# Performance work log

Hardware: AMD Instinct MI355X
Metric: run time of the kernel (lower is better)

Reference implementation:

```python
import jax, jax.numpy as jnp
import numpy as np

B, S, D, H, HS = 2, 2048, 1024, 16, 64


def setup_inputs() -> dict:
    key = jax.random.key(0)
    ks = jax.random.split(key, 4)
    x = jax.random.normal(ks[0], (B, S, D), dtype=jnp.float32)
    # causal mask: 1.0 where key_pos <= query_pos, else 0.0
    mask = jnp.tril(jnp.ones((S, S), dtype=jnp.float32))
    w_qkv = jax.random.normal(ks[1], (D, 3, H, HS), dtype=jnp.float32) * 0.02
    b_qkv = jnp.zeros((3, H, HS), dtype=jnp.float32)
    w_proj = jax.random.normal(ks[2], (H, HS, D), dtype=jnp.float32) * 0.02
    b_proj = jnp.zeros((D,), dtype=jnp.float32)
    return {"x": x, "mask": mask, "w_qkv": w_qkv, "b_qkv": b_qkv,
            "w_proj": w_proj, "b_proj": b_proj}


def reference(x, mask, w_qkv, b_qkv, w_proj, b_proj):
    # c_attn: [B,S,D] @ [D,3,H,HS] -> [B,S,3,H,HS]
    qkv = jnp.einsum('bsd,dthc->bsthc', x, w_qkv) + b_qkv
    q, k, v = qkv[:, :, 0], qkv[:, :, 1], qkv[:, :, 2]  # [B,S,H,HS]
    scale = jax.lax.rsqrt(float(HS))
    q = q * scale
    # scores over head_size: [B,H,S(query),S(key)]
    scores = jnp.einsum('bqhc,bkhc->bhqk', q, k)
    scores = scores + (1.0 - mask) * -1e9
    weights = jax.nn.softmax(scores, axis=-1).astype(x.dtype)
    # attn_pdrop = 0.0 / inference: dropout is identity
    attn = jnp.einsum('bhqk,bkhc->bqhc', weights, v)  # [B,S,H,HS]
    out = jnp.einsum('bqhc,hcd->bqd', attn, w_proj) + b_proj
    return out
```

## Files before the change

### kernel.cpp

```cpp
#include <hip/hip_runtime.h>
#include <hip/hip_bf16.h>


#define Bb 2
#define Ss 2048
#define Dd 1024
#define Hh 16
#define HSs 64

typedef __bf16 bf16x8 __attribute__((ext_vector_type(8)));
typedef float  f32x4  __attribute__((ext_vector_type(4)));

__device__ __forceinline__ unsigned short f2bf(float f) {
  unsigned int u = __float_as_uint(f);
  unsigned int lsb = (u >> 16) & 1u;
  u += 0x7fffu + lsb;
  return (unsigned short)(u >> 16);
}

__device__ __forceinline__ void async16(const unsigned short* g, unsigned short* l) {
  __builtin_amdgcn_global_load_lds(
      (const __attribute__((address_space(1))) unsigned int*)g,
      (__attribute__((address_space(3))) unsigned int*)l,
      16, 0, 0);
}

__global__ __launch_bounds__(256) void k_cvt_bf16(const float* __restrict__ in,
                                                  unsigned short* __restrict__ out,
                                                  int n) {
  int i = (blockIdx.x * 256 + threadIdx.x) * 4;
  int stride = gridDim.x * 256 * 4;
  for (; i < n; i += stride) {
    float4 v = *reinterpret_cast<const float4*>(in + i);
    ushort4 o;
    o.x = f2bf(v.x); o.y = f2bf(v.y); o.z = f2bf(v.z); o.w = f2bf(v.w);
    *reinterpret_cast<ushort4*>(out + i) = o;
  }
}

__global__ __launch_bounds__(256) void k_transpose_bf16(const float* __restrict__ in,
                                                        unsigned short* __restrict__ out,
                                                        int R, int C) {
  __shared__ float t[32][33];
  int c0 = blockIdx.x * 32, r0 = blockIdx.y * 32;
  int tx = threadIdx.x, ty = threadIdx.y;
  #pragma unroll
  for (int i = 0; i < 32; i += 8)
    t[ty + i][tx] = in[(size_t)(r0 + ty + i) * C + (c0 + tx)];
  __syncthreads();
  #pragma unroll
  for (int i = 0; i < 32; i += 8)
    out[(size_t)(c0 + ty + i) * R + (r0 + tx)] = f2bf(t[tx][ty + i]);
}

__global__ __launch_bounds__(256) void k_gemm_qkv(const unsigned short* __restrict__ A,
                                                  const unsigned short* __restrict__ Bt,
                                                  const float* __restrict__ bias,
                                                  unsigned short* __restrict__ Qg,
                                                  unsigned short* __restrict__ Kg,
                                                  unsigned short* __restrict__ Vt) {
  __shared__ unsigned short As[128 * 64];
  __shared__ unsigned short Bs[128 * 64];
  const int K = 1024;
  int bid = blockIdx.x;
  int tm = bid / 24, tn = bid % 24;
  int m0 = tm * 128, n0 = tn * 128;
  int tid = threadIdx.x;
  int w = tid >> 6, l = tid & 63;
  int lr = l & 15, lg = l >> 4;
  int wm = (w >> 1) * 64, wn = (w & 1) * 64;
  int srow = l >> 3, scol = (l & 7) * 8;

  f32x4 acc[4][4];
  #pragma unroll
  for (int i = 0; i < 4; ++i)
    #pragma unroll
    for (int j = 0; j < 4; ++j)
      acc[i][j] = (f32x4){0.f, 0.f, 0.f, 0.f};

  for (int k0 = 0; k0 < K; k0 += 64) {
    #pragma unroll
    for (int c = 0; c < 4; ++c) {
      int chunk = w * 4 + c;
      int row = chunk * 8 + srow;
      async16(&A[(size_t)(m0 + row) * K + k0 + scol], &As[chunk * 512]);
      async16(&Bt[(size_t)(n0 + row) * K + k0 + scol], &Bs[chunk * 512]);
    }
    __syncthreads();
    #pragma unroll
    for (int kk = 0; kk < 64; kk += 32) {
      bf16x8 af[4], bfr[4];
      #pragma unroll
      for (int mf = 0; mf < 4; ++mf)
        af[mf] = *reinterpret_cast<const bf16x8*>(&As[(wm + mf * 16 + lr) * 64 + kk + lg * 8]);
      #pragma unroll
      for (int nf = 0; nf < 4; ++nf)
        bfr[nf] = *reinterpret_cast<const bf16x8*>(&Bs[(wn + nf * 16 + lr) * 64 + kk + lg * 8]);
      #pragma unroll
      for (int mf = 0; mf < 4; ++mf)
        #pragma unroll
        for (int nf = 0; nf < 4; ++nf)
          acc[mf][nf] = __builtin_amdgcn_mfma_f32_16x16x32_bf16(af[mf], bfr[nf], acc[mf][nf], 0, 0, 0);
    }
    __syncthreads();
  }

  #pragma unroll
  for (int mf = 0; mf < 4; ++mf) {
    #pragma unroll
    for (int nf = 0; nf < 4; ++nf) {
      int n = n0 + wn + nf * 16 + lr;
      int t = n >> 10, r = n & 1023;
      int h = r >> 6, cc = r & 63;
      float bv = bias[n];
      if (t == 2) {
        int m = m0 + wm + mf * 16 + lg * 4;
        int b = m >> 11, s = m & 2047;
        ushort4 pk;
        pk.x = f2bf(acc[mf][nf][0] + bv);
        pk.y = f2bf(acc[mf][nf][1] + bv);
        pk.z = f2bf(acc[mf][nf][2] + bv);
        pk.w = f2bf(acc[mf][nf][3] + bv);
        *reinterpret_cast<ushort4*>(&Vt[((size_t)(b * Hh + h) * HSs + cc) * Ss + s]) = pk;
      } else {
        #pragma unroll
        for (int j = 0; j < 4; ++j) {
          int m = m0 + wm + mf * 16 + lg * 4 + j;
          int b = m >> 11, s = m & 2047;
          size_t idx = ((size_t)(b * Hh + h) * Ss + s) * HSs + cc;
          float v = acc[mf][nf][j] + bv;
          if (t == 0) Qg[idx] = f2bf(v * 0.125f);
          else        Kg[idx] = f2bf(v);
        }
      }
    }
  }
}

__global__ __launch_bounds__(256, 4) void k_attn(const unsigned short* __restrict__ Qg,
                                                 const unsigned short* __restrict__ Kg,
                                                 const unsigned short* __restrict__ Vt,
                                                 unsigned short* __restrict__ Ob) {
  __shared__ unsigned short Ks[64 * 64];
  __shared__ unsigned short Vs[64 * 64];
  __shared__ unsigned short Ps[4][16 * 72];

  int bid = blockIdx.x;
  int xcd = bid & 7, slot = (bid >> 3) & 3, idx = bid >> 5;
  int bh = (idx & 3) * 8 + xcd;
  int base = (idx >> 2) * 2 + (slot & 1);
  int qt = (slot & 2) ? 31 - base : base;
  int b = bh >> 4, h = bh & 15;
  int qs0 = qt * 64;

  int tid = threadIdx.x;
  int w = tid >> 6, l = tid & 63;
  int lr = l & 15, lg = l >> 4;
  int qw = qs0 + w * 16;
  int srow = l >> 3, scol = (l & 7) * 8;
  int swcol = scol ^ (srow << 3);

  bf16x8 qf[2];
  #pragma unroll
  for (int kx = 0; kx < 2; ++kx)
    qf[kx] = *reinterpret_cast<const bf16x8*>(
        &Qg[((size_t)bh * Ss + qw + lr) * HSs + kx * 32 + lg * 8]);

  f32x4 oacc[4];
  #pragma unroll
  for (int nf = 0; nf < 4; ++nf) oacc[nf] = (f32x4){0.f, 0.f, 0.f, 0.f};
  float mrun[4], lrun[4];
  #pragma unroll
  for (int j = 0; j < 4; ++j) { mrun[j] = -1e30f; lrun[j] = 0.f; }

  int ntiles = qt + 1;
  for (int t = 0; t < ntiles; ++t) {
    #pragma unroll
    for (int cch = 0; cch < 2; ++cch) {
      int chunk = w * 2 + cch;
      int row = chunk * 8 + srow;
      async16(&Kg[((size_t)bh * Ss + t * 64 + row) * HSs + swcol], &Ks[chunk * 512]);
      async16(&Vt[((size_t)bh * HSs + row) * Ss + t * 64 + swcol], &Vs[chunk * 512]);
    }
    __syncthreads();

    f32x4 sacc[4];
    #pragma unroll
    for (int nf = 0; nf < 4; ++nf) sacc[nf] = (f32x4){0.f, 0.f, 0.f, 0.f};
    #pragma unroll
    for (int kx = 0; kx < 2; ++kx) {
      bf16x8 kf[4];
      #pragma unroll
      for (int nf = 0; nf < 4; ++nf)
        kf[nf] = *reinterpret_cast<const bf16x8*>(
            &Ks[(nf * 16 + lr) * 64 + ((kx * 32 + lg * 8) ^ ((lr & 7) << 3))]);
      #pragma unroll
      for (int nf = 0; nf < 4; ++nf)
        sacc[nf] = __builtin_amdgcn_mfma_f32_16x16x32_bf16(qf[kx], kf[nf], sacc[nf], 0, 0, 0);
    }

    if (t == ntiles - 1) {
      #pragma unroll
      for (int nf = 0; nf < 4; ++nf) {
        int kcol = qs0 + nf * 16 + lr;
        #pragma unroll
        for (int j = 0; j < 4; ++j) {
          int qg = qw + lg * 4 + j;
          if (kcol > qg) sacc[nf][j] = -1e30f;
        }
      }
    }

    #pragma unroll
    for (int j = 0; j < 4; ++j) {
      float rmax = fmaxf(fmaxf(sacc[0][j], sacc[1][j]), fmaxf(sacc[2][j], sacc[3][j]));
      #pragma unroll
      for (int d = 1; d < 16; d <<= 1)
        rmax = fmaxf(rmax, __shfl_xor(rmax, d));
      float mnew = fmaxf(mrun[j], rmax);
      float cf = __expf(mrun[j] - mnew);
      mrun[j] = mnew;
      float psum = 0.f;
      #pragma unroll
      for (int nf = 0; nf < 4; ++nf) {
        float p = __expf(sacc[nf][j] - mnew);
        sacc[nf][j] = p;
        psum += p;
      }
      #pragma unroll
      for (int d = 1; d < 16; d <<= 1)
        psum += __shfl_xor(psum, d);
      lrun[j] = lrun[j] * cf + psum;
      #pragma unroll
      for (int nf = 0; nf < 4; ++nf)
        oacc[nf][j] *= cf;
    }

    #pragma unroll
    for (int nf = 0; nf < 4; ++nf)
      #pragma unroll
      for (int j = 0; j < 4; ++j)
        Ps[w][(lg * 4 + j) * 72 + nf * 16 + lr] = f2bf(sacc[nf][j]);

    #pragma unroll
    for (int kx = 0; kx < 2; ++kx) {
      bf16x8 pf = *reinterpret_cast<const bf16x8*>(&Ps[w][lr * 72 + kx * 32 + lg * 8]);
      bf16x8 vf[4];
      #pragma unroll
      for (int nf = 0; nf < 4; ++nf)
        vf[nf] = *reinterpret_cast<const bf16x8*>(
            &Vs[(nf * 16 + lr) * 64 + ((kx * 32 + lg * 8) ^ ((lr & 7) << 3))]);
      #pragma unroll
      for (int nf = 0; nf < 4; ++nf)
        oacc[nf] = __builtin_amdgcn_mfma_f32_16x16x32_bf16(pf, vf[nf], oacc[nf], 0, 0, 0);
    }
    __syncthreads();
  }

  #pragma unroll
  for (int j = 0; j < 4; ++j) {
    float rinv = 1.0f / lrun[j];
    int s = qw + lg * 4 + j;
    #pragma unroll
    for (int nf = 0; nf < 4; ++nf) {
      int c = nf * 16 + lr;
      Ob[((size_t)(b * Ss + s)) * Dd + h * HSs + c] = f2bf(oacc[nf][j] * rinv);
    }
  }
}

__global__ __launch_bounds__(256) void k_gemm_out(const unsigned short* __restrict__ A,
                                                  const unsigned short* __restrict__ Bt,
                                                  const float* __restrict__ bias,
                                                  float* __restrict__ Out) {
  __shared__ unsigned short As[128 * 64];
  __shared__ unsigned short Bs[128 * 64];
  const int K = 1024;
  int bid = blockIdx.x;
  int tm = bid / 8, tn = bid % 8;
  int m0 = tm * 128, n0 = tn * 128;
  int tid = threadIdx.x;
  int w = tid >> 6, l = tid & 63;
  int lr = l & 15, lg = l >> 4;
  int wm = (w >> 1) * 64, wn = (w & 1) * 64;
  int srow = l >> 3, scol = (l & 7) * 8;

  f32x4 acc[4][4];
  #pragma unroll
  for (int i = 0; i < 4; ++i)
    #pragma unroll
    for (int j = 0; j < 4; ++j)
      acc[i][j] = (f32x4){0.f, 0.f, 0.f, 0.f};

  for (int k0 = 0; k0 < K; k0 += 64) {
    #pragma unroll
    for (int c = 0; c < 4; ++c) {
      int chunk = w * 4 + c;
      int row = chunk * 8 + srow;
      async16(&A[(size_t)(m0 + row) * K + k0 + scol], &As[chunk * 512]);
      async16(&Bt[(size_t)(n0 + row) * K + k0 + scol], &Bs[chunk * 512]);
    }
    __syncthreads();
    #pragma unroll
    for (int kk = 0; kk < 64; kk += 32) {
      bf16x8 af[4], bfr[4];
      #pragma unroll
      for (int mf = 0; mf < 4; ++mf)
        af[mf] = *reinterpret_cast<const bf16x8*>(&As[(wm + mf * 16 + lr) * 64 + kk + lg * 8]);
      #pragma unroll
      for (int nf = 0; nf < 4; ++nf)
        bfr[nf] = *reinterpret_cast<const bf16x8*>(&Bs[(wn + nf * 16 + lr) * 64 + kk + lg * 8]);
      #pragma unroll
      for (int mf = 0; mf < 4; ++mf)
        #pragma unroll
        for (int nf = 0; nf < 4; ++nf)
          acc[mf][nf] = __builtin_amdgcn_mfma_f32_16x16x32_bf16(af[mf], bfr[nf], acc[mf][nf], 0, 0, 0);
    }
    __syncthreads();
  }

  #pragma unroll
  for (int mf = 0; mf < 4; ++mf)
    #pragma unroll
    for (int nf = 0; nf < 4; ++nf) {
      int n = n0 + wn + nf * 16 + lr;
      float bv = bias[n];
      #pragma unroll
      for (int j = 0; j < 4; ++j) {
        int m = m0 + wm + mf * 16 + lg * 4 + j;
        Out[(size_t)m * 1024 + n] = acc[mf][nf][j] + bv;
      }
    }
}

extern "C" void kernel_launch(void* const* d_in, const int* in_sizes, int n_in,
                              void* d_out, int out_size, void* d_ws, size_t ws_size,
                              hipStream_t stream) {
  (void)in_sizes; (void)n_in; (void)out_size; (void)ws_size;
  const float* x      = (const float*)d_in[0];
  const float* w_qkv  = (const float*)d_in[2];
  const float* b_qkv  = (const float*)d_in[3];
  const float* w_proj = (const float*)d_in[4];
  const float* b_proj = (const float*)d_in[5];
  float* out = (float*)d_out;

  char* ws = (char*)d_ws;
  unsigned short* xb    = (unsigned short*)(ws);
  unsigned short* wqkvT = (unsigned short*)(ws + 8388608);
  unsigned short* wpT   = (unsigned short*)(ws + 14680064);
  unsigned short* Qg    = (unsigned short*)(ws + 16777216);
  unsigned short* Kg    = (unsigned short*)(ws + 25165824);
  unsigned short* Vt    = (unsigned short*)(ws + 33554432);
  unsigned short* attnb = (unsigned short*)(ws + 41943040);

  k_cvt_bf16<<<dim3(2048), dim3(256), 0, stream>>>(x, xb, Bb * Ss * Dd);
  k_transpose_bf16<<<dim3(96, 32), dim3(32, 8), 0, stream>>>(w_qkv, wqkvT, 1024, 3072);
  k_transpose_bf16<<<dim3(32, 32), dim3(32, 8), 0, stream>>>(w_proj, wpT, 1024, 1024);
  k_gemm_qkv<<<dim3(32 * 24), dim3(256), 0, stream>>>(xb, wqkvT, b_qkv, Qg, Kg, Vt);
  k_attn<<<dim3(1024), dim3(256), 0, stream>>>(Qg, Kg, Vt, attnb);
  k_gemm_out<<<dim3(32 * 8), dim3(256), 0, stream>>>(attnb, wpT, b_proj, out);
}
```

Baseline: 256.5 us.

## Pair causal query tiles per block with double-buffered K/V and XCD-swizzled GEMMs

The attention kernel now uses 512-thread blocks. Each block's two 4-wave groups handle complementary query tiles (p and 31-p), so every block runs an equal 32-p iterations and the K/V tiles loaded into LDS are shared by both groups. K/V loads are double-buffered so the next tile's async load overlaps the current tile's compute. Both GEMM kernels also remap block IDs so consecutive tiles land on the same XCD for L2 reuse. The cost is doubled LDS use, idle waves in the group whose tile finishes early, and a barrier shared by both groups.

```diff
diff --git a/kernel.cpp b/kernel.cpp
--- a/kernel.cpp
+++ b/kernel.cpp
@@ -63,7 +63,8 @@
   __shared__ unsigned short Bs[128 * 64];
   const int K = 1024;
   int bid = blockIdx.x;
-  int tm = bid / 24, tn = bid % 24;
+  int swz = (bid % 8) * 96 + bid / 8;
+  int tm = swz / 24, tn = swz % 24;
   int m0 = tm * 128, n0 = tn * 128;
   int tid = threadIdx.x;
   int w = tid >> 6, l = tid & 63;
@@ -137,26 +138,26 @@
   }
 }
 
-__global__ __launch_bounds__(256, 4) void k_attn(const unsigned short* __restrict__ Qg,
+__global__ __launch_bounds__(512, 4) void k_attn(const unsigned short* __restrict__ Qg,
                                                  const unsigned short* __restrict__ Kg,
                                                  const unsigned short* __restrict__ Vt,
                                                  unsigned short* __restrict__ Ob) {
-  __shared__ unsigned short Ks[64 * 64];
-  __shared__ unsigned short Vs[64 * 64];
-  __shared__ unsigned short Ps[4][16 * 72];
+  __shared__ unsigned short Ks[2][64 * 64];
+  __shared__ unsigned short Vs[2][64 * 64];
+  __shared__ unsigned short Ps[8][16 * 72];
 
   int bid = blockIdx.x;
-  int xcd = bid & 7, slot = (bid >> 3) & 3, idx = bid >> 5;
-  int bh = (idx & 3) * 8 + xcd;
-  int base = (idx >> 2) * 2 + (slot & 1);
-  int qt = (slot & 2) ? 31 - base : base;
+  int p  = bid >> 5;
+  int bh = bid & 31;
   int b = bh >> 4, h = bh & 15;
-  int qs0 = qt * 64;
 
   int tid = threadIdx.x;
   int w = tid >> 6, l = tid & 63;
+  int g = w >> 2;
+  int myqt = g ? (31 - p) : p;
+  int qs0 = myqt * 64;
   int lr = l & 15, lg = l >> 4;
-  int qw = qs0 + w * 16;
+  int qw = qs0 + (w & 3) * 16;
   int srow = l >> 3, scol = (l & 7) * 8;
   int swcol = scol ^ (srow << 3);
 
@@ -173,86 +174,93 @@
   #pragma unroll
   for (int j = 0; j < 4; ++j) { mrun[j] = -1e30f; lrun[j] = 0.f; }
 
-  int ntiles = qt + 1;
+  int ntiles = 32 - p;
+  {
+    int row = w * 8 + srow;
+    async16(&Kg[((size_t)bh * Ss + 0 * 64 + row) * HSs + swcol], &Ks[0][w * 512]);
+    async16(&Vt[((size_t)bh * HSs + row) * Ss + 0 * 64 + swcol], &Vs[0][w * 512]);
+  }
+  __syncthreads();
+
   for (int t = 0; t < ntiles; ++t) {
-    #pragma unroll
-    for (int cch = 0; cch < 2; ++cch) {
-      int chunk = w * 2 + cch;
-      int row = chunk * 8 + srow;
-      async16(&Kg[((size_t)bh * Ss + t * 64 + row) * HSs + swcol], &Ks[chunk * 512]);
-      async16(&Vt[((size_t)bh * HSs + row) * Ss + t * 64 + swcol], &Vs[chunk * 512]);
-    }
-    __syncthreads();
-
-    f32x4 sacc[4];
-    #pragma unroll
-    for (int nf = 0; nf < 4; ++nf) sacc[nf] = (f32x4){0.f, 0.f, 0.f, 0.f};
-    #pragma unroll
-    for (int kx = 0; kx < 2; ++kx) {
-      bf16x8 kf[4];
+    int cur = t & 1;
+    if (t + 1 < ntiles) {
+      int row = w * 8 + srow;
+      async16(&Kg[((size_t)bh * Ss + (t + 1) * 64 + row) * HSs + swcol], &Ks[cur ^ 1][w * 512]);
+      async16(&Vt[((size_t)bh * HSs + row) * Ss + (t + 1) * 64 + swcol], &Vs[cur ^ 1][w * 512]);
+    }
+
+    if (t <= myqt) {
+      f32x4 sacc[4];
+      #pragma unroll
+      for (int nf = 0; nf < 4; ++nf) sacc[nf] = (f32x4){0.f, 0.f, 0.f, 0.f};
+      #pragma unroll
+      for (int kx = 0; kx < 2; ++kx) {
+        bf16x8 kf[4];
+        #pragma unroll
+        for (int nf = 0; nf < 4; ++nf)
+          kf[nf] = *reinterpret_cast<const bf16x8*>(
+              &Ks[cur][(nf * 16 + lr) * 64 + ((kx * 32 + lg * 8) ^ ((lr & 7) << 3))]);
+        #pragma unroll
+        for (int nf = 0; nf < 4; ++nf)
+          sacc[nf] = __builtin_amdgcn_mfma_f32_16x16x32_bf16(qf[kx], kf[nf], sacc[nf], 0, 0, 0);
+      }
+
+      if (t == myqt) {
+        #pragma unroll
+        for (int nf = 0; nf < 4; ++nf) {
+          int kcol = qs0 + nf * 16 + lr;
+          #pragma unroll
+          for (int j = 0; j < 4; ++j) {
+            int qg2 = qw + lg * 4 + j;
+            if (kcol > qg2) sacc[nf][j] = -1e30f;
+          }
+        }
+      }
+
+      #pragma unroll
+      for (int j = 0; j < 4; ++j) {
+        float rmax = fmaxf(fmaxf(sacc[0][j], sacc[1][j]), fmaxf(sacc[2][j], sacc[3][j]));
+        #pragma unroll
+        for (int d = 1; d < 16; d <<= 1)
+          rmax = fmaxf(rmax, __shfl_xor(rmax, d));
+        float mnew = fmaxf(mrun[j], rmax);
+        float cf = __expf(mrun[j] - mnew);
+        mrun[j] = mnew;
+        float psum = 0.f;
+        #pragma unroll
+        for (int nf = 0; nf < 4; ++nf) {
+          float pv = __expf(sacc[nf][j] - mnew);
+          sacc[nf][j] = pv;
+          psum += pv;
+        }
+        #pragma unroll
+        for (int d = 1; d < 16; d <<= 1)
+          psum += __shfl_xor(psum, d);
+        lrun[j] = lrun[j] * cf + psum;
+        #pragma unroll
+        for (int nf = 0; nf < 4; ++nf)
+          oacc[nf][j] *= cf;
+      }
+
       #pragma unroll
       for (int nf = 0; nf < 4; ++nf)
-        kf[nf] = *reinterpret_cast<const bf16x8*>(
-            &Ks[(nf * 16 + lr) * 64 + ((kx * 32 + lg * 8) ^ ((lr & 7) << 3))]);
-      #pragma unroll
-      for (int nf = 0; nf < 4; ++nf)
-        sacc[nf] = __builtin_amdgcn_mfma_f32_16x16x32_bf16(qf[kx], kf[nf], sacc[nf], 0, 0, 0);
-    }
-
-    if (t == ntiles - 1) {
-      #pragma unroll
-      for (int nf = 0; nf < 4; ++nf) {
-        int kcol = qs0 + nf * 16 + lr;
-        #pragma unroll
-        for (int j = 0; j < 4; ++j) {
-          int qg = qw + lg * 4 + j;
-          if (kcol > qg) sacc[nf][j] = -1e30f;
-        }
-      }
-    }
-
-    #pragma unroll
-    for (int j = 0; j < 4; ++j) {
-      float rmax = fmaxf(fmaxf(sacc[0][j], sacc[1][j]), fmaxf(sacc[2][j], sacc[3][j]));
-      #pragma unroll
-      for (int d = 1; d < 16; d <<= 1)
-        rmax = fmaxf(rmax, __shfl_xor(rmax, d));
-      float mnew = fmaxf(mrun[j], rmax);
-      float cf = __expf(mrun[j] - mnew);
-      mrun[j] = mnew;
-      float psum = 0.f;
-      #pragma unroll
-      for (int nf = 0; nf < 4; ++nf) {
-        float p = __expf(sacc[nf][j] - mnew);
-        sacc[nf][j] = p;
-        psum += p;
-      }
-      #pragma unroll
-      for (int d = 1; d < 16; d <<= 1)
-        psum += __shfl_xor(psum, d);
-      lrun[j] = lrun[j] * cf + psum;
-      #pragma unroll
-      for (int nf = 0; nf < 4; ++nf)
-        oacc[nf][j] *= cf;
-    }
-
-    #pragma unroll
-    for (int nf = 0; nf < 4; ++nf)
-      #pragma unroll
-      for (int j = 0; j < 4; ++j)
-        Ps[w][(lg * 4 + j) * 72 + nf * 16 + lr] = f2bf(sacc[nf][j]);
-
-    #pragma unroll
-    for (int kx = 0; kx < 2; ++kx) {
-      bf16x8 pf = *reinterpret_cast<const bf16x8*>(&Ps[w][lr * 72 + kx * 32 + lg * 8]);
-      bf16x8 vf[4];
-      #pragma unroll
-      for (int nf = 0; nf < 4; ++nf)
-        vf[nf] = *reinterpret_cast<const bf16x8*>(
-            &Vs[(nf * 16 + lr) * 64 + ((kx * 32 + lg * 8) ^ ((lr & 7) << 3))]);
-      #pragma unroll
-      for (int nf = 0; nf < 4; ++nf)
-        oacc[nf] = __builtin_amdgcn_mfma_f32_16x16x32_bf16(pf, vf[nf], oacc[nf], 0, 0, 0);
+        #pragma unroll
+        for (int j = 0; j < 4; ++j)
+          Ps[w][(lg * 4 + j) * 72 + nf * 16 + lr] = f2bf(sacc[nf][j]);
+
+      #pragma unroll
+      for (int kx = 0; kx < 2; ++kx) {
+        bf16x8 pf = *reinterpret_cast<const bf16x8*>(&Ps[w][lr * 72 + kx * 32 + lg * 8]);
+        bf16x8 vf[4];
+        #pragma unroll
+        for (int nf = 0; nf < 4; ++nf)
+          vf[nf] = *reinterpret_cast<const bf16x8*>(
+              &Vs[cur][(nf * 16 + lr) * 64 + ((kx * 32 + lg * 8) ^ ((lr & 7) << 3))]);
+        #pragma unroll
+        for (int nf = 0; nf < 4; ++nf)
+          oacc[nf] = __builtin_amdgcn_mfma_f32_16x16x32_bf16(pf, vf[nf], oacc[nf], 0, 0, 0);
+      }
     }
     __syncthreads();
   }
@@ -277,7 +285,8 @@
   __shared__ unsigned short Bs[128 * 64];
   const int K = 1024;
   int bid = blockIdx.x;
-  int tm = bid / 8, tn = bid % 8;
+  int swz = (bid % 8) * 32 + bid / 8;
+  int tm = swz / 8, tn = swz % 8;
   int m0 = tm * 128, n0 = tn * 128;
   int tid = threadIdx.x;
   int w = tid >> 6, l = tid & 63;
@@ -357,6 +366,6 @@
   k_transpose_bf16<<<dim3(96, 32), dim3(32, 8), 0, stream>>>(w_qkv, wqkvT, 1024, 3072);
   k_transpose_bf16<<<dim3(32, 32), dim3(32, 8), 0, stream>>>(w_proj, wpT, 1024, 1024);
   k_gemm_qkv<<<dim3(32 * 24), dim3(256), 0, stream>>>(xb, wqkvT, b_qkv, Qg, Kg, Vt);
-  k_attn<<<dim3(1024), dim3(256), 0, stream>>>(Qg, Kg, Vt, attnb);
+  k_attn<<<dim3(512), dim3(512), 0, stream>>>(Qg, Kg, Vt, attnb);
   k_gemm_out<<<dim3(32 * 8), dim3(256), 0, stream>>>(attnb, wpT, b_proj, out);
 }
```

New measurement: 237.1 us. 1.08x faster.
